# Kernel optimization log

Hardware: AMD Instinct MI355X
Metric: run time of the kernel (lower is better)

The kernel has to match this reference:

```python
import jax, jax.numpy as jnp
import numpy as np

EMBED_DIM = 1280
NUM_HEADS = 16
PROJ_SIZE = 1280
HEAD_DIM = PROJ_SIZE // NUM_HEADS  # 80
ROT_HALF = HEAD_DIM // 2           # 40
SEQ = 2048
BS = 1


def setup_inputs() -> dict:
    key = jax.random.key(0)
    ks = jax.random.split(key, 6)
    x = jax.random.normal(ks[0], (SEQ, BS, EMBED_DIM), dtype=jnp.float32)
    rotary_pos_emb = jax.random.normal(ks[1], (SEQ, ROT_HALF), dtype=jnp.float32)
    # four equal-length image segments
    cu_seqlens = jnp.array([0, 512, 1024, 1536, 2048], dtype=jnp.int32)
    qkv_w = jax.random.normal(ks[2], (3 * PROJ_SIZE, EMBED_DIM), dtype=jnp.float32) * (EMBED_DIM ** -0.5)
    qkv_b = jnp.zeros((3 * PROJ_SIZE,), dtype=jnp.float32)
    proj_w = jax.random.normal(ks[3], (EMBED_DIM, PROJ_SIZE), dtype=jnp.float32) * (PROJ_SIZE ** -0.5)
    proj_b = jnp.zeros((EMBED_DIM,), dtype=jnp.float32)
    return {"x": x, "rotary_pos_emb": rotary_pos_emb, "cu_seqlens": cu_seqlens,
            "max_seqlen": 512, "qkv_w": qkv_w, "qkv_b": qkv_b,
            "proj_w": proj_w, "proj_b": proj_b}


def _apply_rotary(t, cos, sin):
    # t: [b, s, h, d]; cos/sin: [s, r] with rotary dim = 2r (here 2r == d)
    r = cos.shape[-1]
    cos = cos[None, :, None, :]
    sin = sin[None, :, None, :]
    t1, t2, rest = t[..., :r], t[..., r:2 * r], t[..., 2 * r:]
    rot = jnp.concatenate([t1 * cos - t2 * sin, t2 * cos + t1 * sin], axis=-1)
    return jnp.concatenate([rot, rest], axis=-1) if rest.shape[-1] else rot


def reference(x, rotary_pos_emb, cu_seqlens, max_seqlen, qkv_w, qkv_b, proj_w, proj_b):
    s, b, _ = x.shape
    qkv = x @ qkv_w.T + qkv_b                      # [s, b, 3*H*D]
    q, k, v = jnp.split(qkv, 3, axis=2)
    # [s, b, H, D] -> [b, s, H, D]
    q, k, v = (t.reshape(s, b, NUM_HEADS, HEAD_DIM).transpose(1, 0, 2, 3) for t in (q, k, v))
    cos, sin = jnp.cos(rotary_pos_emb), jnp.sin(rotary_pos_emb)
    q = _apply_rotary(q, cos, sin)
    k = _apply_rotary(k, cos, sin)
    # varlen attention: tokens attend only within their cu_seqlens segment
    pos = jnp.arange(s)
    seg = jnp.searchsorted(cu_seqlens[1:], pos, side='right')  # [s]
    mask = seg[:, None] == seg[None, :]                        # [s, s]
    scale = HEAD_DIM ** -0.5
    scores = jnp.einsum('bshd,bthd->bhst', q, k) * scale       # [b, H, s, s]
    scores = jnp.where(mask[None, None], scores, jnp.finfo(scores.dtype).min)
    probs = jax.nn.softmax(scores, axis=-1)
    out = jnp.einsum('bhst,bthd->bshd', probs, v)              # [b, s, H, D]
    ctx = out.transpose(1, 0, 2, 3).reshape(s, b, PROJ_SIZE)   # [s, b, H*D]
    return ctx @ proj_w.T + proj_b                             # [s, b, embed_dim]
```

## Files before the change

kernel.cpp:

```cpp
#include <hip/hip_runtime.h>
#include <hip/hip_bf16.h>
#include <cstdint>
#include <cstddef>

#define EMBED 1280
#define NHEAD 16
#define HD 80
#define ROT 40
#define SEQL 2048
#define QKV_N 3840
#define QKV_STRIDE (NHEAD * SEQL * HD)

typedef __attribute__((ext_vector_type(8))) short short8v;
typedef __attribute__((ext_vector_type(4))) short short4v;
typedef __attribute__((ext_vector_type(4))) float f32x4;

__device__ inline unsigned short f2bf(float f) {
    unsigned u = __float_as_uint(f);
    u += 0x7FFFu + ((u >> 16) & 1u);
    return (unsigned short)(u >> 16);
}
__device__ inline float bf2f(unsigned short h) {
    return __uint_as_float(((unsigned)h) << 16);
}

__global__ __launch_bounds__(256) void split_bf16_kernel(
    const float* __restrict__ src, unsigned short* __restrict__ hi,
    unsigned short* __restrict__ lo, int n4)
{
    int i = blockIdx.x * 256 + threadIdx.x;
    if (i >= n4) return;
    float4 v = reinterpret_cast<const float4*>(src)[i];
    unsigned short h0 = f2bf(v.x), h1 = f2bf(v.y), h2 = f2bf(v.z), h3 = f2bf(v.w);
    short4v hv, lv;
    hv[0] = (short)h0; hv[1] = (short)h1; hv[2] = (short)h2; hv[3] = (short)h3;
    lv[0] = (short)f2bf(v.x - bf2f(h0));
    lv[1] = (short)f2bf(v.y - bf2f(h1));
    lv[2] = (short)f2bf(v.z - bf2f(h2));
    lv[3] = (short)f2bf(v.w - bf2f(h3));
    *reinterpret_cast<short4v*>(&hi[i * 4]) = hv;
    *reinterpret_cast<short4v*>(&lo[i * 4]) = lv;
}

template <int MODE>
__global__ __launch_bounds__(256) void gemm_mfma_kernel(
    const float* __restrict__ A, const float* __restrict__ B,
    const float* __restrict__ bias, float* __restrict__ C,
    int M, int N, int K)
{
    __shared__ unsigned short As[2 * 128 * 32];
    __shared__ unsigned short Bs[2 * 128 * 32];

    const int tid  = threadIdx.x;
    const int m0   = blockIdx.y * 128;
    const int n0   = blockIdx.x * 128;
    const int wave = tid >> 6;
    const int lane = tid & 63;
    const int wm   = (wave >> 1) * 64;
    const int wn   = (wave & 1) * 64;
    const int lrow = lane & 15;
    const int lg   = lane >> 4;

    f32x4 acc[4][4];
#pragma unroll
    for (int i = 0; i < 4; ++i)
#pragma unroll
        for (int j = 0; j < 4; ++j) acc[i][j] = (f32x4){0.f, 0.f, 0.f, 0.f};

    for (int k0 = 0; k0 < K; k0 += 32) {
        float4 ar[4], br[4];
#pragma unroll
        for (int l = 0; l < 4; ++l) {
            int id = l * 256 + tid;
            int r = id >> 3, c = id & 7;
            ar[l] = *reinterpret_cast<const float4*>(&A[(size_t)(m0 + r) * K + k0 + c * 4]);
            br[l] = *reinterpret_cast<const float4*>(&B[(size_t)(n0 + r) * K + k0 + c * 4]);
        }
        __syncthreads();
#pragma unroll
        for (int l = 0; l < 4; ++l) {
            int id = l * 256 + tid;
            int r = id >> 3, c = id & 7;
            int base = r * 32 + (((c >> 1) ^ (r & 3)) << 3) + ((c & 1) << 2);
            float4 v = ar[l];
            unsigned short h0 = f2bf(v.x), h1 = f2bf(v.y), h2 = f2bf(v.z), h3 = f2bf(v.w);
            unsigned short g0 = f2bf(v.x - bf2f(h0)), g1 = f2bf(v.y - bf2f(h1));
            unsigned short g2 = f2bf(v.z - bf2f(h2)), g3 = f2bf(v.w - bf2f(h3));
            uint2 w;
            w.x = (unsigned)h0 | ((unsigned)h1 << 16); w.y = (unsigned)h2 | ((unsigned)h3 << 16);
            *reinterpret_cast<uint2*>(&As[base]) = w;
            w.x = (unsigned)g0 | ((unsigned)g1 << 16); w.y = (unsigned)g2 | ((unsigned)g3 << 16);
            *reinterpret_cast<uint2*>(&As[4096 + base]) = w;
            v = br[l];
            h0 = f2bf(v.x); h1 = f2bf(v.y); h2 = f2bf(v.z); h3 = f2bf(v.w);
            g0 = f2bf(v.x - bf2f(h0)); g1 = f2bf(v.y - bf2f(h1));
            g2 = f2bf(v.z - bf2f(h2)); g3 = f2bf(v.w - bf2f(h3));
            w.x = (unsigned)h0 | ((unsigned)h1 << 16); w.y = (unsigned)h2 | ((unsigned)h3 << 16);
            *reinterpret_cast<uint2*>(&Bs[base]) = w;
            w.x = (unsigned)g0 | ((unsigned)g1 << 16); w.y = (unsigned)g2 | ((unsigned)g3 << 16);
            *reinterpret_cast<uint2*>(&Bs[4096 + base]) = w;
        }
        __syncthreads();
        short8v bh[4], bl[4];
#pragma unroll
        for (int fn = 0; fn < 4; ++fn) {
            int row = wn + fn * 16 + lrow;
            int idx = row * 32 + ((lg ^ (row & 3)) << 3);
            bh[fn] = *reinterpret_cast<const short8v*>(&Bs[idx]);
            bl[fn] = *reinterpret_cast<const short8v*>(&Bs[4096 + idx]);
        }
#pragma unroll
        for (int fm = 0; fm < 4; ++fm) {
            int row = wm + fm * 16 + lrow;
            int idx = row * 32 + ((lg ^ (row & 3)) << 3);
            short8v ah = *reinterpret_cast<const short8v*>(&As[idx]);
            short8v al = *reinterpret_cast<const short8v*>(&As[4096 + idx]);
#pragma unroll
            for (int fn = 0; fn < 4; ++fn) {
                acc[fm][fn] = __builtin_amdgcn_mfma_f32_16x16x32_bf16(ah, bh[fn], acc[fm][fn], 0, 0, 0);
                acc[fm][fn] = __builtin_amdgcn_mfma_f32_16x16x32_bf16(ah, bl[fn], acc[fm][fn], 0, 0, 0);
                acc[fm][fn] = __builtin_amdgcn_mfma_f32_16x16x32_bf16(al, bh[fn], acc[fm][fn], 0, 0, 0);
            }
        }
    }

#pragma unroll
    for (int fn = 0; fn < 4; ++fn) {
        int n = n0 + wn + fn * 16 + lrow;
        float bcol = bias[n];
        if (MODE == 0) {
#pragma unroll
            for (int fm = 0; fm < 4; ++fm) {
#pragma unroll
                for (int q = 0; q < 4; ++q) {
                    int m = m0 + wm + fm * 16 + lg * 4 + q;
                    C[(size_t)m * N + n] = acc[fm][fn][q] + bcol;
                }
            }
        } else {
            int part = n / EMBED;
            int rem  = n - part * EMBED;
            int head = rem / HD;
            int d    = rem - head * HD;
            float* dst = C + (size_t)part * QKV_STRIDE + (size_t)head * SEQL * HD + d;
#pragma unroll
            for (int fm = 0; fm < 4; ++fm) {
#pragma unroll
                for (int q = 0; q < 4; ++q) {
                    int m = m0 + wm + fm * 16 + lg * 4 + q;
                    dst[(size_t)m * HD] = acc[fm][fn][q] + bcol;
                }
            }
        }
    }
}

template <int MODE>
__global__ __launch_bounds__(256) void gemm_mfma_pre_kernel(
    const unsigned short* __restrict__ Ah, const unsigned short* __restrict__ Al,
    const unsigned short* __restrict__ Bh, const unsigned short* __restrict__ Bl,
    const float* __restrict__ bias, float* __restrict__ C,
    int M, int N, int K)
{
    __shared__ unsigned short As[2 * 128 * 32];
    __shared__ unsigned short Bs[2 * 128 * 32];

    const int tid  = threadIdx.x;
    const int m0   = blockIdx.y * 128;
    const int n0   = blockIdx.x * 128;
    const int wave = tid >> 6;
    const int lane = tid & 63;
    const int wm   = (wave >> 1) * 64;
    const int wn   = (wave & 1) * 64;
    const int lrow = lane & 15;
    const int lg   = lane >> 4;

    f32x4 acc[4][4];
#pragma unroll
    for (int i = 0; i < 4; ++i)
#pragma unroll
        for (int j = 0; j < 4; ++j) acc[i][j] = (f32x4){0.f, 0.f, 0.f, 0.f};

    for (int k0 = 0; k0 < K; k0 += 32) {
        short8v rah[2], ral[2], rbh[2], rbl[2];
#pragma unroll
        for (int l = 0; l < 2; ++l) {
            int id = l * 256 + tid;
            int r = id >> 2, b = id & 3;
            size_t offA = (size_t)(m0 + r) * K + k0 + b * 8;
            size_t offB = (size_t)(n0 + r) * K + k0 + b * 8;
            rah[l] = *reinterpret_cast<const short8v*>(&Ah[offA]);
            ral[l] = *reinterpret_cast<const short8v*>(&Al[offA]);
            rbh[l] = *reinterpret_cast<const short8v*>(&Bh[offB]);
            rbl[l] = *reinterpret_cast<const short8v*>(&Bl[offB]);
        }
        __syncthreads();
#pragma unroll
        for (int l = 0; l < 2; ++l) {
            int id = l * 256 + tid;
            int r = id >> 2, b = id & 3;
            int base = r * 32 + ((b ^ (r & 3)) << 3);
            *reinterpret_cast<short8v*>(&As[base]) = rah[l];
            *reinterpret_cast<short8v*>(&As[4096 + base]) = ral[l];
            *reinterpret_cast<short8v*>(&Bs[base]) = rbh[l];
            *reinterpret_cast<short8v*>(&Bs[4096 + base]) = rbl[l];
        }
        __syncthreads();
        short8v bh[4], bl[4];
#pragma unroll
        for (int fn = 0; fn < 4; ++fn) {
            int row = wn + fn * 16 + lrow;
            int idx = row * 32 + ((lg ^ (row & 3)) << 3);
            bh[fn] = *reinterpret_cast<const short8v*>(&Bs[idx]);
            bl[fn] = *reinterpret_cast<const short8v*>(&Bs[4096 + idx]);
        }
#pragma unroll
        for (int fm = 0; fm < 4; ++fm) {
            int row = wm + fm * 16 + lrow;
            int idx = row * 32 + ((lg ^ (row & 3)) << 3);
            short8v ah = *reinterpret_cast<const short8v*>(&As[idx]);
            short8v al = *reinterpret_cast<const short8v*>(&As[4096 + idx]);
#pragma unroll
            for (int fn = 0; fn < 4; ++fn) {
                acc[fm][fn] = __builtin_amdgcn_mfma_f32_16x16x32_bf16(ah, bh[fn], acc[fm][fn], 0, 0, 0);
                acc[fm][fn] = __builtin_amdgcn_mfma_f32_16x16x32_bf16(ah, bl[fn], acc[fm][fn], 0, 0, 0);
                acc[fm][fn] = __builtin_amdgcn_mfma_f32_16x16x32_bf16(al, bh[fn], acc[fm][fn], 0, 0, 0);
            }
        }
    }

#pragma unroll
    for (int fn = 0; fn < 4; ++fn) {
        int n = n0 + wn + fn * 16 + lrow;
        float bcol = bias[n];
        if (MODE == 0) {
#pragma unroll
            for (int fm = 0; fm < 4; ++fm) {
#pragma unroll
                for (int q = 0; q < 4; ++q) {
                    int m = m0 + wm + fm * 16 + lg * 4 + q;
                    C[(size_t)m * N + n] = acc[fm][fn][q] + bcol;
                }
            }
        } else {
            int part = n / EMBED;
            int rem  = n - part * EMBED;
            int head = rem / HD;
            int d    = rem - head * HD;
            float* dst = C + (size_t)part * QKV_STRIDE + (size_t)head * SEQL * HD + d;
#pragma unroll
            for (int fm = 0; fm < 4; ++fm) {
#pragma unroll
                for (int q = 0; q < 4; ++q) {
                    int m = m0 + wm + fm * 16 + lg * 4 + q;
                    dst[(size_t)m * HD] = acc[fm][fn][q] + bcol;
                }
            }
        }
    }
}

__global__ __launch_bounds__(256) void rotary_kernel(
    float* __restrict__ Q, float* __restrict__ K, const float* __restrict__ rpe)
{
    int idx = blockIdx.x * 256 + threadIdx.x;
    int r = idx % ROT;
    int s = (idx / ROT) & (SEQL - 1);
    int h = (idx / (ROT * SEQL)) & (NHEAD - 1);
    float* buf = (idx >= NHEAD * SEQL * ROT) ? K : Q;
    float* p = buf + ((size_t)h * SEQL + s) * HD;
    float ang = rpe[s * ROT + r];
    float c = cosf(ang), sn = sinf(ang);
    float t1 = p[r], t2 = p[r + ROT];
    p[r]       = t1 * c - t2 * sn;
    p[r + ROT] = t2 * c + t1 * sn;
}

#define KSTR 104
#define VSTR 72
#define PSTR 72

__global__ __launch_bounds__(256) void attn_mfma_kernel(
    const float* __restrict__ Qb, const float* __restrict__ Kb,
    const float* __restrict__ Vb, const int* __restrict__ cu, int nseg,
    float* __restrict__ ctx)
{
    __shared__ unsigned short kv_hi[64 * KSTR];
    __shared__ unsigned short kv_lo[64 * KSTR];
    __shared__ unsigned short p_hi[64 * PSTR];
    __shared__ unsigned short p_lo[64 * PSTR];

    const int tid  = threadIdx.x;
    const int lane = tid & 63;
    const int wave = tid >> 6;
    const int lg   = lane >> 4;
    const int col  = lane & 15;
    const int h    = blockIdx.y;
    const int r0   = blockIdx.x * 64;
    const int wrow = wave * 16;

    int qstart[4], qend[4];
#pragma unroll
    for (int q = 0; q < 4; ++q) {
        int row = r0 + wrow + lg * 4 + q;
        int sid = 0;
        for (int i = 1; i <= nseg; ++i) sid += (cu[i] <= row);
        qstart[q] = (sid == 0) ? 0 : cu[sid];
        qend[q]   = (sid >= nseg) ? SEQL : cu[sid + 1];
    }
    int blo, bhi;
    {
        int sid = 0;
        for (int i = 1; i <= nseg; ++i) sid += (cu[i] <= r0);
        blo = (sid == 0) ? 0 : cu[sid];
        sid = 0;
        for (int i = 1; i <= nseg; ++i) sid += (cu[i] <= r0 + 63);
        bhi = (sid >= nseg) ? SEQL : cu[sid + 1];
    }

    const float scale = 0.11180339887498949f;
    short8v qh[3], qlo[3];
    {
        const float* Qr = Qb + ((size_t)h * SEQL + r0 + wrow + col) * HD;
#pragma unroll
        for (int kc = 0; kc < 3; ++kc) {
            int d0 = kc * 32 + lg * 8;
            float v[8];
            if (d0 < HD) {
                float4 f0 = *reinterpret_cast<const float4*>(&Qr[d0]);
                float4 f1 = *reinterpret_cast<const float4*>(&Qr[d0 + 4]);
                v[0] = f0.x * scale; v[1] = f0.y * scale; v[2] = f0.z * scale; v[3] = f0.w * scale;
                v[4] = f1.x * scale; v[5] = f1.y * scale; v[6] = f1.z * scale; v[7] = f1.w * scale;
            } else {
#pragma unroll
                for (int j = 0; j < 8; ++j) v[j] = 0.f;
            }
            short8v hh, ll;
#pragma unroll
            for (int j = 0; j < 8; ++j) {
                unsigned short hb = f2bf(v[j]);
                hh[j] = (short)hb;
                ll[j] = (short)f2bf(v[j] - bf2f(hb));
            }
            qh[kc] = hh; qlo[kc] = ll;
        }
    }

    f32x4 oacc[5];
#pragma unroll
    for (int fn = 0; fn < 5; ++fn) oacc[fn] = (f32x4){0.f, 0.f, 0.f, 0.f};
    float mrun[4] = {-1e30f, -1e30f, -1e30f, -1e30f};
    float lrun[4] = {0.f, 0.f, 0.f, 0.f};

    const float* Kh = Kb + (size_t)h * SEQL * HD;
    const float* Vh = Vb + (size_t)h * SEQL * HD;

    for (int kb = (blo & ~63); kb < bhi; kb += 64) {
        __syncthreads();

        const float* Kt = Kh + (size_t)kb * HD;
#pragma unroll
        for (int l = 0; l < 5; ++l) {
            int idx = tid + l * 256;
            int ky = idx / 20, fc = idx % 20;
            float4 f = *reinterpret_cast<const float4*>(&Kt[ky * HD + fc * 4]);
            int base = ky * KSTR + fc * 4;
            unsigned short h0 = f2bf(f.x), h1 = f2bf(f.y), h2 = f2bf(f.z), h3 = f2bf(f.w);
            uint2 w;
            w.x = (unsigned)h0 | ((unsigned)h1 << 16); w.y = (unsigned)h2 | ((unsigned)h3 << 16);
            *reinterpret_cast<uint2*>(&kv_hi[base]) = w;
            h0 = f2bf(f.x - bf2f(h0)); h1 = f2bf(f.y - bf2f(h1));
            h2 = f2bf(f.z - bf2f(h2)); h3 = f2bf(f.w - bf2f(h3));
            w.x = (unsigned)h0 | ((unsigned)h1 << 16); w.y = (unsigned)h2 | ((unsigned)h3 << 16);
            *reinterpret_cast<uint2*>(&kv_lo[base]) = w;
        }
        {
            int ky = tid >> 2, off = (tid & 3) << 2;
            uint2 z; z.x = 0u; z.y = 0u;
            *reinterpret_cast<uint2*>(&kv_hi[ky * KSTR + 80 + off]) = z;
            *reinterpret_cast<uint2*>(&kv_lo[ky * KSTR + 80 + off]) = z;
        }
        __syncthreads();

        f32x4 sfr[4];
#pragma unroll
        for (int kt = 0; kt < 4; ++kt) {
            f32x4 s = (f32x4){0.f, 0.f, 0.f, 0.f};
#pragma unroll
            for (int kc = 0; kc < 3; ++kc) {
                int bidx = (kt * 16 + col) * KSTR + kc * 32 + lg * 8;
                short8v kh = *reinterpret_cast<const short8v*>(&kv_hi[bidx]);
                short8v kl = *reinterpret_cast<const short8v*>(&kv_lo[bidx]);
                s = __builtin_amdgcn_mfma_f32_16x16x32_bf16(qh[kc],  kh, s, 0, 0, 0);
                s = __builtin_amdgcn_mfma_f32_16x16x32_bf16(qlo[kc], kh, s, 0, 0, 0);
                s = __builtin_amdgcn_mfma_f32_16x16x32_bf16(qh[kc],  kl, s, 0, 0, 0);
            }
            sfr[kt] = s;
        }
        __syncthreads();

        const float* Vt = Vh + (size_t)kb * HD;
        float4 vreg[5];
#pragma unroll
        for (int l = 0; l < 5; ++l) {
            int idx = tid + l * 256;
            int fc = idx >> 6, ky = idx & 63;
            vreg[l] = *reinterpret_cast<const float4*>(&Vt[ky * HD + fc * 4]);
        }

#pragma unroll
        for (int q = 0; q < 4; ++q) {
            float sv[4];
            float mx = -1e30f;
#pragma unroll
            for (int kt = 0; kt < 4; ++kt) {
                int key = kb + kt * 16 + col;
                bool ok = (key >= qstart[q]) && (key < qend[q]);
                sv[kt] = ok ? sfr[kt][q] : -1e30f;
                mx = fmaxf(mx, sv[kt]);
            }
            mx = fmaxf(mx, __shfl_xor(mx, 1));
            mx = fmaxf(mx, __shfl_xor(mx, 2));
            mx = fmaxf(mx, __shfl_xor(mx, 4));
            mx = fmaxf(mx, __shfl_xor(mx, 8));
            float mnew  = fmaxf(mrun[q], mx);
            float alpha = __expf(mrun[q] - mnew);
            float ps = 0.f;
            int prow = (wrow + lg * 4 + q) * PSTR;
#pragma unroll
            for (int kt = 0; kt < 4; ++kt) {
                float p = (sv[kt] > -1e29f) ? __expf(sv[kt] - mnew) : 0.f;
                ps += p;
                unsigned short ph = f2bf(p);
                p_hi[prow + kt * 16 + col] = ph;
                p_lo[prow + kt * 16 + col] = f2bf(p - bf2f(ph));
            }
            ps += __shfl_xor(ps, 1);
            ps += __shfl_xor(ps, 2);
            ps += __shfl_xor(ps, 4);
            ps += __shfl_xor(ps, 8);
            lrun[q] = lrun[q] * alpha + ps;
            mrun[q] = mnew;
#pragma unroll
            for (int fn = 0; fn < 5; ++fn) oacc[fn][q] *= alpha;
        }

#pragma unroll
        for (int l = 0; l < 5; ++l) {
            int idx = tid + l * 256;
            int fc = idx >> 6, ky = idx & 63;
            float4 f = vreg[l];
            float vv[4] = {f.x, f.y, f.z, f.w};
#pragma unroll
            for (int e = 0; e < 4; ++e) {
                unsigned short hb = f2bf(vv[e]);
                kv_hi[(fc * 4 + e) * VSTR + ky] = hb;
                kv_lo[(fc * 4 + e) * VSTR + ky] = f2bf(vv[e] - bf2f(hb));
            }
        }
        __syncthreads();

#pragma unroll
        for (int kc2 = 0; kc2 < 2; ++kc2) {
            int aidx = (wrow + col) * PSTR + kc2 * 32 + lg * 8;
            short8v pah = *reinterpret_cast<const short8v*>(&p_hi[aidx]);
            short8v pal = *reinterpret_cast<const short8v*>(&p_lo[aidx]);
#pragma unroll
            for (int fn = 0; fn < 5; ++fn) {
                int bidx = (fn * 16 + col) * VSTR + kc2 * 32 + lg * 8;
                short8v vh = *reinterpret_cast<const short8v*>(&kv_hi[bidx]);
                short8v vl = *reinterpret_cast<const short8v*>(&kv_lo[bidx]);
                oacc[fn] = __builtin_amdgcn_mfma_f32_16x16x32_bf16(pah, vh, oacc[fn], 0, 0, 0);
                oacc[fn] = __builtin_amdgcn_mfma_f32_16x16x32_bf16(pal, vh, oacc[fn], 0, 0, 0);
                oacc[fn] = __builtin_amdgcn_mfma_f32_16x16x32_bf16(pah, vl, oacc[fn], 0, 0, 0);
            }
        }
    }

#pragma unroll
    for (int q = 0; q < 4; ++q) {
        float inv = 1.f / lrun[q];
        float* cp = &ctx[(size_t)(r0 + wrow + lg * 4 + q) * EMBED + h * HD];
#pragma unroll
        for (int fn = 0; fn < 5; ++fn)
            cp[fn * 16 + col] = oacc[fn][q] * inv;
    }
}

extern "C" void kernel_launch(void* const* d_in, const int* in_sizes, int n_in,
                              void* d_out, int out_size, void* d_ws, size_t ws_size,
                              hipStream_t stream)
{
    const float* x      = (const float*)d_in[0];
    const float* rpe    = (const float*)d_in[1];
    const int*   cu     = (const int*)d_in[2];
    const float* qkv_w  = (const float*)d_in[4];
    const float* qkv_b  = (const float*)d_in[5];
    const float* proj_w = (const float*)d_in[6];
    const float* proj_b = (const float*)d_in[7];

    float* ws  = (float*)d_ws;
    float* Q   = ws;
    float* K   = ws + (size_t)QKV_STRIDE;
    float* V   = ws + (size_t)2 * QKV_STRIDE;
    float* ctx = ws + (size_t)3 * QKV_STRIDE;

    const int nseg = in_sizes[2] - 1;

    const bool HOIST = ws_size >= 68157440ULL;

    if (HOIST) {
        unsigned short* xh   = (unsigned short*)(ws + (size_t)3 * QKV_STRIDE);
        unsigned short* xl   = xh + (size_t)SEQL * EMBED;
        unsigned short* wh   = (unsigned short*)(ws + (size_t)4 * QKV_STRIDE);
        unsigned short* wl   = wh + (size_t)QKV_N * EMBED;
        unsigned short* ctxh = (unsigned short*)(ws + (size_t)4 * QKV_STRIDE);
        unsigned short* ctxl = ctxh + (size_t)SEQL * EMBED;
        unsigned short* ph   = (unsigned short*)((char*)d_ws + 61603840);
        unsigned short* pl   = ph + (size_t)EMBED * EMBED;

        split_bf16_kernel<<<(SEQL * EMBED / 4 + 255) / 256, 256, 0, stream>>>(x, xh, xl, SEQL * EMBED / 4);
        split_bf16_kernel<<<(QKV_N * EMBED / 4 + 255) / 256, 256, 0, stream>>>(qkv_w, wh, wl, QKV_N * EMBED / 4);
        split_bf16_kernel<<<(EMBED * EMBED / 4 + 255) / 256, 256, 0, stream>>>(proj_w, ph, pl, EMBED * EMBED / 4);

        gemm_mfma_pre_kernel<1><<<dim3(QKV_N / 128, SEQL / 128), 256, 0, stream>>>(
            xh, xl, wh, wl, qkv_b, Q, SEQL, QKV_N, EMBED);

        rotary_kernel<<<(2 * NHEAD * SEQL * ROT) / 256, 256, 0, stream>>>(Q, K, rpe);

        attn_mfma_kernel<<<dim3(SEQL / 64, NHEAD), 256, 0, stream>>>(Q, K, V, cu, nseg, ctx);

        split_bf16_kernel<<<(SEQL * EMBED / 4 + 255) / 256, 256, 0, stream>>>(ctx, ctxh, ctxl, SEQL * EMBED / 4);
        gemm_mfma_pre_kernel<0><<<dim3(EMBED / 128, SEQL / 128), 256, 0, stream>>>(
            ctxh, ctxl, ph, pl, proj_b, (float*)d_out, SEQL, EMBED, EMBED);
    } else {
        gemm_mfma_kernel<1><<<dim3(QKV_N / 128, SEQL / 128), 256, 0, stream>>>(
            x, qkv_w, qkv_b, Q, SEQL, QKV_N, EMBED);
        rotary_kernel<<<(2 * NHEAD * SEQL * ROT) / 256, 256, 0, stream>>>(Q, K, rpe);
        attn_mfma_kernel<<<dim3(SEQL / 64, NHEAD), 256, 0, stream>>>(Q, K, V, cu, nseg, ctx);
        gemm_mfma_kernel<0><<<dim3(EMBED / 128, SEQL / 128), 256, 0, stream>>>(
            ctx, proj_w, proj_b, (float*)d_out, SEQL, EMBED, EMBED);
    }
}
```

Before: 287.8 us.

## Double-buffer pre-split GEMM, fuse ctx split into attention, merge split launches

The pre-split bf16 GEMM now double-buffers its shared-memory tiles. The next K-tile's global loads are issued before the current tile's MFMAs and stored afterwards, which leaves one barrier per step instead of two. The attention kernel writes the context output directly as hi/lo bf16 planes, removing the separate split pass and the fp32 ctx round-trip. The three input split kernels are merged into one launch. The cost is doubled LDS use per GEMM block, which may lower occupancy, and more registers held for prefetch.

```diff
diff --git a/kernel.cpp b/kernel.cpp
--- a/kernel.cpp
+++ b/kernel.cpp
@@ -24,22 +24,27 @@
     return __uint_as_float(((unsigned)h) << 16);
 }
 
-__global__ __launch_bounds__(256) void split_bf16_kernel(
-    const float* __restrict__ src, unsigned short* __restrict__ hi,
-    unsigned short* __restrict__ lo, int n4)
+__global__ __launch_bounds__(256) void split3_kernel(
+    const float* __restrict__ s0, unsigned short* __restrict__ h0, unsigned short* __restrict__ l0, int c0,
+    const float* __restrict__ s1, unsigned short* __restrict__ h1, unsigned short* __restrict__ l1, int c1,
+    const float* __restrict__ s2, unsigned short* __restrict__ h2, unsigned short* __restrict__ l2, int c2)
 {
     int i = blockIdx.x * 256 + threadIdx.x;
-    if (i >= n4) return;
-    float4 v = reinterpret_cast<const float4*>(src)[i];
-    unsigned short h0 = f2bf(v.x), h1 = f2bf(v.y), h2 = f2bf(v.z), h3 = f2bf(v.w);
+    const float* s; unsigned short *hp, *lp; int base;
+    if (i < c0)               { s = s0; hp = h0; lp = l0; base = i; }
+    else if (i < c0 + c1)     { s = s1; hp = h1; lp = l1; base = i - c0; }
+    else if (i < c0 + c1 + c2){ s = s2; hp = h2; lp = l2; base = i - c0 - c1; }
+    else return;
+    float4 v = reinterpret_cast<const float4*>(s)[base];
+    unsigned short a0 = f2bf(v.x), a1 = f2bf(v.y), a2 = f2bf(v.z), a3 = f2bf(v.w);
     short4v hv, lv;
-    hv[0] = (short)h0; hv[1] = (short)h1; hv[2] = (short)h2; hv[3] = (short)h3;
-    lv[0] = (short)f2bf(v.x - bf2f(h0));
-    lv[1] = (short)f2bf(v.y - bf2f(h1));
-    lv[2] = (short)f2bf(v.z - bf2f(h2));
-    lv[3] = (short)f2bf(v.w - bf2f(h3));
-    *reinterpret_cast<short4v*>(&hi[i * 4]) = hv;
-    *reinterpret_cast<short4v*>(&lo[i * 4]) = lv;
+    hv[0] = (short)a0; hv[1] = (short)a1; hv[2] = (short)a2; hv[3] = (short)a3;
+    lv[0] = (short)f2bf(v.x - bf2f(a0));
+    lv[1] = (short)f2bf(v.y - bf2f(a1));
+    lv[2] = (short)f2bf(v.z - bf2f(a2));
+    lv[3] = (short)f2bf(v.w - bf2f(a3));
+    *reinterpret_cast<short4v*>(&hp[base * 4]) = hv;
+    *reinterpret_cast<short4v*>(&lp[base * 4]) = lv;
 }
 
 template <int MODE>
@@ -155,6 +160,56 @@
     }
 }
 
+#define GSTEP(CURBUF, NXTBUF, T, PRE)                                          \
+    {                                                                          \
+        short8v nah[2], nal[2], nbh[2], nbl[2];                                \
+        if (PRE) {                                                             \
+            _Pragma("unroll")                                                  \
+            for (int l = 0; l < 2; ++l) {                                      \
+                int id = l * 256 + tid; int r = id >> 2, b = id & 3;           \
+                size_t offA = (size_t)(m0 + r) * K + (size_t)(T + 1) * 32 + b * 8; \
+                size_t offB = (size_t)(n0 + r) * K + (size_t)(T + 1) * 32 + b * 8; \
+                nah[l] = *reinterpret_cast<const short8v*>(&Ah[offA]);         \
+                nal[l] = *reinterpret_cast<const short8v*>(&Al[offA]);         \
+                nbh[l] = *reinterpret_cast<const short8v*>(&Bh[offB]);         \
+                nbl[l] = *reinterpret_cast<const short8v*>(&Bl[offB]);         \
+            }                                                                  \
+        }                                                                      \
+        short8v fbh[4], fbl[4];                                                \
+        _Pragma("unroll")                                                      \
+        for (int fn = 0; fn < 4; ++fn) {                                       \
+            int row = wn + fn * 16 + lrow;                                     \
+            int idx = row * 32 + ((lg ^ (row & 3)) << 3);                      \
+            fbh[fn] = *reinterpret_cast<const short8v*>(&Bs[CURBUF][idx]);     \
+            fbl[fn] = *reinterpret_cast<const short8v*>(&Bs[CURBUF][4096 + idx]); \
+        }                                                                      \
+        _Pragma("unroll")                                                      \
+        for (int fm = 0; fm < 4; ++fm) {                                       \
+            int row = wm + fm * 16 + lrow;                                     \
+            int idx = row * 32 + ((lg ^ (row & 3)) << 3);                      \
+            short8v ah = *reinterpret_cast<const short8v*>(&As[CURBUF][idx]);  \
+            short8v al = *reinterpret_cast<const short8v*>(&As[CURBUF][4096 + idx]); \
+            _Pragma("unroll")                                                  \
+            for (int fn = 0; fn < 4; ++fn) {                                   \
+                acc[fm][fn] = __builtin_amdgcn_mfma_f32_16x16x32_bf16(ah, fbh[fn], acc[fm][fn], 0, 0, 0); \
+                acc[fm][fn] = __builtin_amdgcn_mfma_f32_16x16x32_bf16(ah, fbl[fn], acc[fm][fn], 0, 0, 0); \
+                acc[fm][fn] = __builtin_amdgcn_mfma_f32_16x16x32_bf16(al, fbh[fn], acc[fm][fn], 0, 0, 0); \
+            }                                                                  \
+        }                                                                      \
+        if (PRE) {                                                             \
+            _Pragma("unroll")                                                  \
+            for (int l = 0; l < 2; ++l) {                                      \
+                int id = l * 256 + tid; int r = id >> 2, b = id & 3;           \
+                int base = r * 32 + ((b ^ (r & 3)) << 3);                      \
+                *reinterpret_cast<short8v*>(&As[NXTBUF][base]) = nah[l];       \
+                *reinterpret_cast<short8v*>(&As[NXTBUF][4096 + base]) = nal[l];\
+                *reinterpret_cast<short8v*>(&Bs[NXTBUF][base]) = nbh[l];       \
+                *reinterpret_cast<short8v*>(&Bs[NXTBUF][4096 + base]) = nbl[l];\
+            }                                                                  \
+            __syncthreads();                                                   \
+        }                                                                      \
+    }
+
 template <int MODE>
 __global__ __launch_bounds__(256) void gemm_mfma_pre_kernel(
     const unsigned short* __restrict__ Ah, const unsigned short* __restrict__ Al,
@@ -162,8 +217,8 @@
     const float* __restrict__ bias, float* __restrict__ C,
     int M, int N, int K)
 {
-    __shared__ unsigned short As[2 * 128 * 32];
-    __shared__ unsigned short Bs[2 * 128 * 32];
+    __shared__ unsigned short As[2][2 * 128 * 32];
+    __shared__ unsigned short Bs[2][2 * 128 * 32];
 
     const int tid  = threadIdx.x;
     const int m0   = blockIdx.y * 128;
@@ -181,52 +236,27 @@
 #pragma unroll
         for (int j = 0; j < 4; ++j) acc[i][j] = (f32x4){0.f, 0.f, 0.f, 0.f};
 
-    for (int k0 = 0; k0 < K; k0 += 32) {
-        short8v rah[2], ral[2], rbh[2], rbl[2];
-#pragma unroll
-        for (int l = 0; l < 2; ++l) {
-            int id = l * 256 + tid;
-            int r = id >> 2, b = id & 3;
-            size_t offA = (size_t)(m0 + r) * K + k0 + b * 8;
-            size_t offB = (size_t)(n0 + r) * K + k0 + b * 8;
-            rah[l] = *reinterpret_cast<const short8v*>(&Ah[offA]);
-            ral[l] = *reinterpret_cast<const short8v*>(&Al[offA]);
-            rbh[l] = *reinterpret_cast<const short8v*>(&Bh[offB]);
-            rbl[l] = *reinterpret_cast<const short8v*>(&Bl[offB]);
-        }
-        __syncthreads();
-#pragma unroll
-        for (int l = 0; l < 2; ++l) {
-            int id = l * 256 + tid;
-            int r = id >> 2, b = id & 3;
-            int base = r * 32 + ((b ^ (r & 3)) << 3);
-            *reinterpret_cast<short8v*>(&As[base]) = rah[l];
-            *reinterpret_cast<short8v*>(&As[4096 + base]) = ral[l];
-            *reinterpret_cast<short8v*>(&Bs[base]) = rbh[l];
-            *reinterpret_cast<short8v*>(&Bs[4096 + base]) = rbl[l];
-        }
-        __syncthreads();
-        short8v bh[4], bl[4];
-#pragma unroll
-        for (int fn = 0; fn < 4; ++fn) {
-            int row = wn + fn * 16 + lrow;
-            int idx = row * 32 + ((lg ^ (row & 3)) << 3);
-            bh[fn] = *reinterpret_cast<const short8v*>(&Bs[idx]);
-            bl[fn] = *reinterpret_cast<const short8v*>(&Bs[4096 + idx]);
-        }
-#pragma unroll
-        for (int fm = 0; fm < 4; ++fm) {
-            int row = wm + fm * 16 + lrow;
-            int idx = row * 32 + ((lg ^ (row & 3)) << 3);
-            short8v ah = *reinterpret_cast<const short8v*>(&As[idx]);
-            short8v al = *reinterpret_cast<const short8v*>(&As[4096 + idx]);
-#pragma unroll
-            for (int fn = 0; fn < 4; ++fn) {
-                acc[fm][fn] = __builtin_amdgcn_mfma_f32_16x16x32_bf16(ah, bh[fn], acc[fm][fn], 0, 0, 0);
-                acc[fm][fn] = __builtin_amdgcn_mfma_f32_16x16x32_bf16(ah, bl[fn], acc[fm][fn], 0, 0, 0);
-                acc[fm][fn] = __builtin_amdgcn_mfma_f32_16x16x32_bf16(al, bh[fn], acc[fm][fn], 0, 0, 0);
-            }
-        }
+#pragma unroll
+    for (int l = 0; l < 2; ++l) {
+        int id = l * 256 + tid; int r = id >> 2, b = id & 3;
+        size_t offA = (size_t)(m0 + r) * K + b * 8;
+        size_t offB = (size_t)(n0 + r) * K + b * 8;
+        short8v vah = *reinterpret_cast<const short8v*>(&Ah[offA]);
+        short8v val = *reinterpret_cast<const short8v*>(&Al[offA]);
+        short8v vbh = *reinterpret_cast<const short8v*>(&Bh[offB]);
+        short8v vbl = *reinterpret_cast<const short8v*>(&Bl[offB]);
+        int base = r * 32 + ((b ^ (r & 3)) << 3);
+        *reinterpret_cast<short8v*>(&As[0][base]) = vah;
+        *reinterpret_cast<short8v*>(&As[0][4096 + base]) = val;
+        *reinterpret_cast<short8v*>(&Bs[0][base]) = vbh;
+        *reinterpret_cast<short8v*>(&Bs[0][4096 + base]) = vbl;
+    }
+    __syncthreads();
+
+    const int NT = K >> 5;
+    for (int t = 0; t < NT; t += 2) {
+        GSTEP(0, 1, t, t + 1 < NT);
+        if (t + 1 < NT) GSTEP(1, 0, t + 1, t + 2 < NT);
     }
 
 #pragma unroll
@@ -280,10 +310,12 @@
 #define VSTR 72
 #define PSTR 72
 
+template <int PLANES>
 __global__ __launch_bounds__(256) void attn_mfma_kernel(
     const float* __restrict__ Qb, const float* __restrict__ Kb,
     const float* __restrict__ Vb, const int* __restrict__ cu, int nseg,
-    float* __restrict__ ctx)
+    float* __restrict__ ctx, unsigned short* __restrict__ ctxh,
+    unsigned short* __restrict__ ctxl)
 {
     __shared__ unsigned short kv_hi[64 * KSTR];
     __shared__ unsigned short kv_lo[64 * KSTR];
@@ -480,10 +512,20 @@
 #pragma unroll
     for (int q = 0; q < 4; ++q) {
         float inv = 1.f / lrun[q];
-        float* cp = &ctx[(size_t)(r0 + wrow + lg * 4 + q) * EMBED + h * HD];
-#pragma unroll
-        for (int fn = 0; fn < 5; ++fn)
-            cp[fn * 16 + col] = oacc[fn][q] * inv;
+        size_t rowoff = (size_t)(r0 + wrow + lg * 4 + q) * EMBED + h * HD;
+        if (PLANES) {
+#pragma unroll
+            for (int fn = 0; fn < 5; ++fn) {
+                float val = oacc[fn][q] * inv;
+                unsigned short hb = f2bf(val);
+                ctxh[rowoff + fn * 16 + col] = hb;
+                ctxl[rowoff + fn * 16 + col] = f2bf(val - bf2f(hb));
+            }
+        } else {
+#pragma unroll
+            for (int fn = 0; fn < 5; ++fn)
+                ctx[rowoff + fn * 16 + col] = oacc[fn][q] * inv;
+        }
     }
 }
 
@@ -519,25 +561,27 @@
         unsigned short* ph   = (unsigned short*)((char*)d_ws + 61603840);
         unsigned short* pl   = ph + (size_t)EMBED * EMBED;
 
-        split_bf16_kernel<<<(SEQL * EMBED / 4 + 255) / 256, 256, 0, stream>>>(x, xh, xl, SEQL * EMBED / 4);
-        split_bf16_kernel<<<(QKV_N * EMBED / 4 + 255) / 256, 256, 0, stream>>>(qkv_w, wh, wl, QKV_N * EMBED / 4);
-        split_bf16_kernel<<<(EMBED * EMBED / 4 + 255) / 256, 256, 0, stream>>>(proj_w, ph, pl, EMBED * EMBED / 4);
+        const int c0 = SEQL * EMBED / 4, c1 = QKV_N * EMBED / 4, c2 = EMBED * EMBED / 4;
+
+        split3_kernel<<<(c0 + c1 + c2 + 255) / 256, 256, 0, stream>>>(
+            x, xh, xl, c0, qkv_w, wh, wl, c1, proj_w, ph, pl, c2);
 
         gemm_mfma_pre_kernel<1><<<dim3(QKV_N / 128, SEQL / 128), 256, 0, stream>>>(
             xh, xl, wh, wl, qkv_b, Q, SEQL, QKV_N, EMBED);
 
         rotary_kernel<<<(2 * NHEAD * SEQL * ROT) / 256, 256, 0, stream>>>(Q, K, rpe);
 
-        attn_mfma_kernel<<<dim3(SEQL / 64, NHEAD), 256, 0, stream>>>(Q, K, V, cu, nseg, ctx);
-
-        split_bf16_kernel<<<(SEQL * EMBED / 4 + 255) / 256, 256, 0, stream>>>(ctx, ctxh, ctxl, SEQL * EMBED / 4);
+        attn_mfma_kernel<1><<<dim3(SEQL / 64, NHEAD), 256, 0, stream>>>(
+            Q, K, V, cu, nseg, nullptr, ctxh, ctxl);
+
         gemm_mfma_pre_kernel<0><<<dim3(EMBED / 128, SEQL / 128), 256, 0, stream>>>(
             ctxh, ctxl, ph, pl, proj_b, (float*)d_out, SEQL, EMBED, EMBED);
     } else {
         gemm_mfma_kernel<1><<<dim3(QKV_N / 128, SEQL / 128), 256, 0, stream>>>(
             x, qkv_w, qkv_b, Q, SEQL, QKV_N, EMBED);
         rotary_kernel<<<(2 * NHEAD * SEQL * ROT) / 256, 256, 0, stream>>>(Q, K, rpe);
-        attn_mfma_kernel<<<dim3(SEQL / 64, NHEAD), 256, 0, stream>>>(Q, K, V, cu, nseg, ctx);
+        attn_mfma_kernel<0><<<dim3(SEQL / 64, NHEAD), 256, 0, stream>>>(
+            Q, K, V, cu, nseg, ctx, nullptr, nullptr);
         gemm_mfma_kernel<0><<<dim3(EMBED / 128, SEQL / 128), 256, 0, stream>>>(
             ctx, proj_w, proj_b, (float*)d_out, SEQL, EMBED, EMBED);
     }
```

New measurement: 298.9 us. +3.9%, slower.
